# Kernel optimization log

Measured on AMD Instinct MI355X. Metric: run time of the kernel, lower is better.

The kernel has to match this reference:

```python
import jax, jax.numpy as jnp
import numpy as np


def setup_inputs() -> dict:
    key = jax.random.key(0)
    x = jax.random.normal(key, (64, 128, 10000), dtype=jnp.float32)
    return {"x": x}


def reference(x):
    # x: (batch, channels, time)
    # 1) average reference: subtract mean across channels
    x = x - jnp.mean(x, axis=1, keepdims=True)
    # 2) channel-wise zscore: mean/std over time per channel (ddof=0, like np.std)
    mean = jnp.mean(x, axis=2, keepdims=True)
    std = jnp.std(x, axis=2, keepdims=True)
    std = jnp.where(std == 0, jnp.ones_like(std), std)
    return (x - mean) / std
```

## Files before the change

### kernel.cpp

```cpp
#include <hip/hip_runtime.h>
#include <math.h>


#define BB 64
#define CC 128
#define TT 10000
#define T4 2500

__global__ __launch_bounds__(256) void chmean_kernel(const float4* __restrict__ x,
                                                     float4* __restrict__ m) {
    const int t4 = blockIdx.x * 256 + threadIdx.x;
    const int b = blockIdx.y;
    if (t4 >= T4) return;
    const float4* xb = x + (size_t)b * CC * T4;
    float4 acc = make_float4(0.f, 0.f, 0.f, 0.f);
#pragma unroll 4
    for (int c = 0; c < CC; ++c) {
        float4 v = xb[(size_t)c * T4 + t4];
        acc.x += v.x; acc.y += v.y; acc.z += v.z; acc.w += v.w;
    }
    const float s = 1.0f / (float)CC;
    acc.x *= s; acc.y *= s; acc.z *= s; acc.w *= s;
    m[(size_t)b * T4 + t4] = acc;
}

__global__ __launch_bounds__(256) void zscore_kernel(const float4* __restrict__ x,
                                                     const float4* __restrict__ m,
                                                     float4* __restrict__ out) {
    __shared__ float4 y[T4];
    __shared__ float redS[4], redQ[4];
    __shared__ float s_mean, s_inv;

    const int tid = threadIdx.x;
    const int b = blockIdx.x >> 7;
    const int c = blockIdx.x & 127;

    const float4* xr = x + ((size_t)b * CC + c) * T4;
    const float4* mr = m + (size_t)b * T4;

    float sum = 0.f, sq = 0.f;
    for (int i = tid; i < T4; i += 256) {
        float4 v = xr[i];
        float4 mv = mr[i];
        v.x -= mv.x; v.y -= mv.y; v.z -= mv.z; v.w -= mv.w;
        y[i] = v;
        sum += v.x + v.y + v.z + v.w;
        sq  += v.x * v.x + v.y * v.y + v.z * v.z + v.w * v.w;
    }

#pragma unroll
    for (int off = 32; off > 0; off >>= 1) {
        sum += __shfl_down(sum, off, 64);
        sq  += __shfl_down(sq,  off, 64);
    }
    const int wave = tid >> 6;
    if ((tid & 63) == 0) { redS[wave] = sum; redQ[wave] = sq; }
    __syncthreads();

    if (tid == 0) {
        const float S = redS[0] + redS[1] + redS[2] + redS[3];
        const float Q = redQ[0] + redQ[1] + redQ[2] + redQ[3];
        const float mean = S / (float)TT;
        float var = Q / (float)TT - mean * mean;
        if (var < 0.f) var = 0.f;
        const float sd = sqrtf(var);
        s_mean = mean;
        s_inv = (sd == 0.f) ? 1.f : 1.f / sd;
    }
    __syncthreads();

    const float mean = s_mean, inv = s_inv;
    float4* orow = out + ((size_t)b * CC + c) * T4;
    for (int i = tid; i < T4; i += 256) {
        float4 v = y[i];
        v.x = (v.x - mean) * inv;
        v.y = (v.y - mean) * inv;
        v.z = (v.z - mean) * inv;
        v.w = (v.w - mean) * inv;
        orow[i] = v;
    }
}

extern "C" void kernel_launch(void* const* d_in, const int* in_sizes, int n_in,
                              void* d_out, int out_size, void* d_ws, size_t ws_size,
                              hipStream_t stream) {
    const float4* x = (const float4*)d_in[0];
    float4* out = (float4*)d_out;
    float4* m = (float4*)d_ws;

    dim3 g1((T4 + 255) / 256, BB);
    chmean_kernel<<<g1, 256, 0, stream>>>(x, m);

    zscore_kernel<<<BB * CC, 256, 0, stream>>>(x, m, out);
}
```

Before: 604.8 us.

## Keep zscore row in registers and split channel-mean across waves

The zscore kernel now holds each thread's slice of the row in a fully unrolled float4 register array instead of a 40 KB shared-memory buffer. This removes the LDS footprint that limited resident blocks per CU, at the cost of about 40 extra VGPRs per thread. The channel-mean kernel now splits the 128 channels across four waves per block, each covering 64 time positions, and combines the partial sums through shared memory. That gives the mean pass many more blocks and more loads in flight.

```diff
diff --git a/kernel.cpp b/kernel.cpp
--- a/kernel.cpp
+++ b/kernel.cpp
@@ -6,28 +6,47 @@
 #define CC 128
 #define TT 10000
 #define T4 2500
+#define K2 10
 
 __global__ __launch_bounds__(256) void chmean_kernel(const float4* __restrict__ x,
                                                      float4* __restrict__ m) {
-    const int t4 = blockIdx.x * 256 + threadIdx.x;
-    const int b = blockIdx.y;
-    if (t4 >= T4) return;
+    __shared__ float4 sh[4][64];
+
+    const int tid  = threadIdx.x;
+    const int wave = tid >> 6;
+    const int lane = tid & 63;
+    const int t4   = blockIdx.x * 64 + lane;
+    const int b    = blockIdx.y;
+
     const float4* xb = x + (size_t)b * CC * T4;
+
     float4 acc = make_float4(0.f, 0.f, 0.f, 0.f);
-#pragma unroll 4
-    for (int c = 0; c < CC; ++c) {
-        float4 v = xb[(size_t)c * T4 + t4];
-        acc.x += v.x; acc.y += v.y; acc.z += v.z; acc.w += v.w;
+    if (t4 < T4) {
+        const int c0 = wave * 32;
+#pragma unroll 8
+        for (int cc = 0; cc < 32; ++cc) {
+            float4 v = xb[(size_t)(c0 + cc) * T4 + t4];
+            acc.x += v.x; acc.y += v.y; acc.z += v.z; acc.w += v.w;
+        }
     }
-    const float s = 1.0f / (float)CC;
-    acc.x *= s; acc.y *= s; acc.z *= s; acc.w *= s;
-    m[(size_t)b * T4 + t4] = acc;
+    sh[wave][lane] = acc;
+    __syncthreads();
+
+    if (wave == 0 && t4 < T4) {
+        float4 a0 = sh[0][lane], a1 = sh[1][lane], a2 = sh[2][lane], a3 = sh[3][lane];
+        const float s = 1.0f / (float)CC;
+        float4 r;
+        r.x = (a0.x + a1.x + a2.x + a3.x) * s;
+        r.y = (a0.y + a1.y + a2.y + a3.y) * s;
+        r.z = (a0.z + a1.z + a2.z + a3.z) * s;
+        r.w = (a0.w + a1.w + a2.w + a3.w) * s;
+        m[(size_t)b * T4 + t4] = r;
+    }
 }
 
 __global__ __launch_bounds__(256) void zscore_kernel(const float4* __restrict__ x,
                                                      const float4* __restrict__ m,
                                                      float4* __restrict__ out) {
-    __shared__ float4 y[T4];
     __shared__ float redS[4], redQ[4];
     __shared__ float s_mean, s_inv;
 
@@ -38,14 +57,19 @@
     const float4* xr = x + ((size_t)b * CC + c) * T4;
     const float4* mr = m + (size_t)b * T4;
 
+    float4 yv[K2];
     float sum = 0.f, sq = 0.f;
-    for (int i = tid; i < T4; i += 256) {
-        float4 v = xr[i];
-        float4 mv = mr[i];
-        v.x -= mv.x; v.y -= mv.y; v.z -= mv.z; v.w -= mv.w;
-        y[i] = v;
-        sum += v.x + v.y + v.z + v.w;
-        sq  += v.x * v.x + v.y * v.y + v.z * v.z + v.w * v.w;
+#pragma unroll
+    for (int k = 0; k < K2; ++k) {
+        const int i = tid + k * 256;
+        if (i < T4) {
+            float4 v  = xr[i];
+            float4 mv = mr[i];
+            v.x -= mv.x; v.y -= mv.y; v.z -= mv.z; v.w -= mv.w;
+            yv[k] = v;
+            sum += v.x + v.y + v.z + v.w;
+            sq  += v.x * v.x + v.y * v.y + v.z * v.z + v.w * v.w;
+        }
     }
 
 #pragma unroll
@@ -71,13 +95,17 @@
 
     const float mean = s_mean, inv = s_inv;
     float4* orow = out + ((size_t)b * CC + c) * T4;
-    for (int i = tid; i < T4; i += 256) {
-        float4 v = y[i];
-        v.x = (v.x - mean) * inv;
-        v.y = (v.y - mean) * inv;
-        v.z = (v.z - mean) * inv;
-        v.w = (v.w - mean) * inv;
-        orow[i] = v;
+#pragma unroll
+    for (int k = 0; k < K2; ++k) {
+        const int i = tid + k * 256;
+        if (i < T4) {
+            float4 v = yv[k];
+            v.x = (v.x - mean) * inv;
+            v.y = (v.y - mean) * inv;
+            v.z = (v.z - mean) * inv;
+            v.w = (v.w - mean) * inv;
+            orow[i] = v;
+        }
     }
 }
 
@@ -88,7 +116,7 @@
     float4* out = (float4*)d_out;
     float4* m = (float4*)d_ws;
 
-    dim3 g1((T4 + 255) / 256, BB);
+    dim3 g1((T4 + 63) / 64, BB);
     chmean_kernel<<<g1, 256, 0, stream>>>(x, m);
 
     zscore_kernel<<<BB * CC, 256, 0, stream>>>(x, m, out);
```

Result: no change. 598.4 us (-1.1%).
